# Kernel optimization log

Hardware: AMD Instinct MI355X
Metric: run time of the kernel (lower is better)

Reference implementation:

```python
import jax, jax.numpy as jnp
import numpy as np

B, T, C, NH = 1, 2048, 1024, 16
HS = C // NH            # 64
LEVEL = 6
LMIN = 2 ** LEVEL       # 64 (tail block size)
NB = T // LMIN          # 32 complete sets


def setup_inputs() -> dict:
    key = jax.random.key(0)
    ks = jax.random.split(key, 8)
    def w(k, shape, fan_in):
        return jax.random.normal(k, shape, jnp.float32) / np.sqrt(fan_in)
    return {
        "x": jax.random.normal(ks[0], (B, T, C), jnp.float32),
        "Wq": w(ks[1], (C, C), C),
        "Wk": w(ks[2], (C, C), C),
        "Wv": w(ks[3], (C, C), C),
        "Wkmap": w(ks[4], (HS, HS * HS), HS * HS),
        "bkmap": jnp.zeros((HS,), jnp.float32),
        "Wvmap": w(ks[5], (HS, HS * HS), HS * HS),
        "bvmap": jnp.zeros((HS,), jnp.float32),
        "Wc": w(ks[6], (C, C), C),
        "bc": jnp.zeros((C,), jnp.float32),
    }


def reference(x, Wq, Wk, Wv, Wkmap, bkmap, Wvmap, bvmap, Wc, bc):
    phi = lambda t: jax.nn.elu(t) + 1.0  # feature_map='elu'
    # preprocess: projections + feature map (no q/k normalization)
    q = phi((x @ Wq.T).reshape(B, T, NH, HS))
    k = phi((x @ Wk.T).reshape(B, T, NH, HS))
    v = (x @ Wv.T).reshape(B, T, NH, HS)

    # per-position outer products k_t (x) v_t, grouped into LMIN-sized blocks
    op = jnp.einsum('bthd,bthe->bthde', k, v).reshape(B, NB, LMIN, NH, HS, HS)
    # set feature = final state of linear-attn recurrence over each full block
    set_f = op.sum(axis=2).reshape(B, NB, NH, HS * HS)            # [B,NB,NH,HS^2]
    # tail feature at t = state over [t - t%LMIN, t] = in-block prefix cumsum
    tail_f = jnp.cumsum(op, axis=2).reshape(B, T, NH, HS * HS)    # [B,T,NH,HS^2]

    K = set_f @ Wkmap.T + bkmap      # [B,NB,NH,HS] (k_mapping=True)
    V = set_f @ Wvmap.T + bvmap      # [B,NB,NH,HS] (v_mapping=True)
    K_tail = tail_f @ Wkmap.T + bkmap  # [B,T,NH,HS]
    V_tail = tail_f @ Wvmap.T + bvmap  # [B,T,NH,HS]

    scale = 1.0 / np.sqrt(HS)
    logits = jnp.einsum('bthd,bshd->bhts', q, K) * scale          # [B,NH,T,NB]
    # query t may attend only complete sets strictly before its own block
    mask = jnp.arange(NB)[None, :] < (jnp.arange(T) // LMIN)[:, None]  # [T,NB]
    logits = jnp.where(mask[None, None], logits, -jnp.inf)
    tail_logit = (jnp.einsum('bthd,bthd->bth', q, K_tail) * scale)
    tail_logit = tail_logit.transpose(0, 2, 1)[..., None]         # [B,NH,T,1]

    att = jax.nn.softmax(jnp.concatenate([logits, tail_logit], axis=-1), axis=-1)
    out = (jnp.einsum('bhts,bshd->bhtd', att[..., :-1], V)
           + att[..., -1:] * V_tail.transpose(0, 2, 1, 3))        # [B,NH,T,HS]
    out = out.transpose(0, 2, 1, 3).reshape(B, T, C)
    return out @ Wc.T + bc
```

## Files before the change

kernel.cpp:

```cpp
#include <hip/hip_runtime.h>
#include <hip/hip_bf16.h>
#include <math.h>

typedef __hip_bfloat16 bf16;
typedef __attribute__((ext_vector_type(8))) short short8;
typedef __attribute__((ext_vector_type(4))) float f32x4;

#define C_DIM 1024
#define NHEAD 16
#define HS 64

__device__ __forceinline__ float bf2f(bf16 x) { return __bfloat162float(x); }

__device__ __forceinline__ void split8(const float* p, short8& h, short8& l) {
    float4 f0 = reinterpret_cast<const float4*>(p)[0];
    float4 f1 = reinterpret_cast<const float4*>(p)[1];
    float vals[8] = {f0.x, f0.y, f0.z, f0.w, f1.x, f1.y, f1.z, f1.w};
#pragma unroll
    for (int j = 0; j < 8; ++j) {
        bf16 hb = __float2bfloat16(vals[j]);
        float r = vals[j] - __bfloat162float(hb);
        h[j] = *reinterpret_cast<short*>(&hb);
        bf16 lb = __float2bfloat16(r);
        l[j] = *reinterpret_cast<short*>(&lb);
    }
}

__device__ __forceinline__ short8* tchunk(bf16* tile, int row, int ch) {
    return reinterpret_cast<short8*>(tile + row * 64 + (((ch) ^ (row & 7)) << 3));
}

__global__ __launch_bounds__(256) void presplit_all_kernel(
    const float* __restrict__ x, const float* __restrict__ Wq,
    const float* __restrict__ Wk, const float* __restrict__ Wv,
    bf16* __restrict__ xh, bf16* __restrict__ xl,
    bf16* __restrict__ wqh, bf16* __restrict__ wql,
    bf16* __restrict__ wkh, bf16* __restrict__ wkl,
    bf16* __restrict__ wvh, bf16* __restrict__ wvl)
{
    int blk = blockIdx.x;
    const float* src; bf16 *dh, *dl; long off;
    if (blk < 1024)      { src = x;  dh = xh;  dl = xl;  off = (long)blk * 2048; }
    else if (blk < 1536) { src = Wq; dh = wqh; dl = wql; off = (long)(blk - 1024) * 2048; }
    else if (blk < 2048) { src = Wk; dh = wkh; dl = wkl; off = (long)(blk - 1536) * 2048; }
    else                 { src = Wv; dh = wvh; dl = wvl; off = (long)(blk - 2048) * 2048; }
    long p = off + threadIdx.x * 8;
    short8 h8, l8;
    split8(&src[p], h8, l8);
    *reinterpret_cast<short8*>(&dh[p]) = h8;
    *reinterpret_cast<short8*>(&dl[p]) = l8;
}

__global__ __launch_bounds__(256) void presplit_wc_kernel(
    const float* __restrict__ Wc, bf16* __restrict__ wch, bf16* __restrict__ wcl)
{
    long p = (long)blockIdx.x * 2048 + threadIdx.x * 8;
    short8 h8, l8;
    split8(&Wc[p], h8, l8);
    *reinterpret_cast<short8*>(&wch[p]) = h8;
    *reinterpret_cast<short8*>(&wcl[p]) = l8;
}

__global__ __launch_bounds__(256) void presplit_wmap_kernel(
    const float* __restrict__ WK, const float* __restrict__ WV, bf16* __restrict__ Wm4)
{
    int d = blockIdx.x;
    int row = threadIdx.x >> 2, e0 = (threadIdx.x & 3) * 16;
    const float* pk = &WK[(long)row * 4096 + d * 64 + e0];
    const float* pv = &WV[(long)row * 4096 + d * 64 + e0];
    long bKh = (((long)(d * 4 + 0) * 64) + row) * 64 + e0;
    long bKl = (((long)(d * 4 + 1) * 64) + row) * 64 + e0;
    long bVh = (((long)(d * 4 + 2) * 64) + row) * 64 + e0;
    long bVl = (((long)(d * 4 + 3) * 64) + row) * 64 + e0;
    short8 h8, l8;
    split8(pk, h8, l8);     *(short8*)&Wm4[bKh] = h8;     *(short8*)&Wm4[bKl] = l8;
    split8(pk + 8, h8, l8); *(short8*)&Wm4[bKh + 8] = h8; *(short8*)&Wm4[bKl + 8] = l8;
    split8(pv, h8, l8);     *(short8*)&Wm4[bVh] = h8;     *(short8*)&Wm4[bVl] = l8;
    split8(pv + 8, h8, l8); *(short8*)&Wm4[bVh + 8] = h8; *(short8*)&Wm4[bVl + 8] = l8;
}

__global__ __launch_bounds__(256) void qkv_kernel(
    const bf16* __restrict__ xh, const bf16* __restrict__ xl,
    const bf16* __restrict__ wqh, const bf16* __restrict__ wql,
    const bf16* __restrict__ wkh, const bf16* __restrict__ wkl,
    const bf16* __restrict__ wvh, const bf16* __restrict__ wvl,
    float* __restrict__ qkv)
{
    __shared__ bf16 Ah[8192], Al[8192], Bh[8192], Bl[8192];
    const int tid = threadIdx.x;
    const int lane = tid & 63, wid = tid >> 6;
    const int wr = wid >> 1, wc = wid & 1;
    const int proj = blockIdx.x >> 3;
    const int n0 = (blockIdx.x & 7) * 128;
    const int m0 = blockIdx.y * 128;
    const bf16* Bhp = proj == 0 ? wqh : (proj == 1 ? wkh : wvh);
    const bf16* Blp = proj == 0 ? wql : (proj == 1 ? wkl : wvl);
    float* C = qkv + (long)proj * 2097152;

    f32x4 acc[4][4] = {};
    for (int kt = 0; kt < 16; ++kt) {
        const int k0 = kt << 6;
#pragma unroll
        for (int i = 0; i < 4; ++i) {
            int cc = tid + i * 256;
            int row = cc >> 3, ch = cc & 7;
            *tchunk(Ah, row, ch) = *(const short8*)&xh[(long)(m0 + row) * 1024 + k0 + ch * 8];
            *tchunk(Al, row, ch) = *(const short8*)&xl[(long)(m0 + row) * 1024 + k0 + ch * 8];
            *tchunk(Bh, row, ch) = *(const short8*)&Bhp[(long)(n0 + row) * 1024 + k0 + ch * 8];
            *tchunk(Bl, row, ch) = *(const short8*)&Blp[(long)(n0 + row) * 1024 + k0 + ch * 8];
        }
        __syncthreads();
#pragma unroll
        for (int kk = 0; kk < 2; ++kk) {
            short8 afh[4], afl[4], bfh[4], bfl[4];
#pragma unroll
            for (int t = 0; t < 4; ++t) {
                int ra = wr * 64 + t * 16 + (lane & 15);
                int rb = wc * 64 + t * 16 + (lane & 15);
                int ch = kk * 4 + (lane >> 4);
                afh[t] = *tchunk(Ah, ra, ch);
                afl[t] = *tchunk(Al, ra, ch);
                bfh[t] = *tchunk(Bh, rb, ch);
                bfl[t] = *tchunk(Bl, rb, ch);
            }
#pragma unroll
            for (int tm = 0; tm < 4; ++tm)
#pragma unroll
                for (int tn = 0; tn < 4; ++tn) {
                    acc[tm][tn] = __builtin_amdgcn_mfma_f32_16x16x32_bf16(
                        afh[tm], bfh[tn], acc[tm][tn], 0, 0, 0);
                    acc[tm][tn] = __builtin_amdgcn_mfma_f32_16x16x32_bf16(
                        afh[tm], bfl[tn], acc[tm][tn], 0, 0, 0);
                    acc[tm][tn] = __builtin_amdgcn_mfma_f32_16x16x32_bf16(
                        afl[tm], bfh[tn], acc[tm][tn], 0, 0, 0);
                }
        }
        __syncthreads();
    }
#pragma unroll
    for (int tm = 0; tm < 4; ++tm)
#pragma unroll
        for (int tn = 0; tn < 4; ++tn)
#pragma unroll
            for (int r = 0; r < 4; ++r) {
                int row = m0 + wr * 64 + tm * 16 + (lane >> 4) * 4 + r;
                int col = n0 + wc * 64 + tn * 16 + (lane & 15);
                float v = acc[tm][tn][r];
                if (proj < 2) v = v > 0.f ? v + 1.f : __expf(v);
                C[(long)row * 1024 + col] = v;
            }
}

__global__ __launch_bounds__(256) void setfeat_kernel(
    const float* __restrict__ kbuf, const float* __restrict__ vbuf,
    const bf16* __restrict__ Wm4,
    const float* __restrict__ bkmap, const float* __restrict__ bvmap,
    float* __restrict__ Ktail, float* __restrict__ Vtail,
    float* __restrict__ Kset, float* __restrict__ Vset)
{
    __shared__ char smem[49152];
    bf16* Wt = reinterpret_cast<bf16*>(smem);
    float* kT = reinterpret_cast<float*>(smem + 32768);
    float(*WallK)[64] = reinterpret_cast<float(*)[64]>(smem);
    float(*WallV)[64] = reinterpret_cast<float(*)[64]>(smem + 16384);

    const int tid = threadIdx.x;
    const int lane = tid & 63, wid = tid >> 6;
    const int wr = wid >> 1, wc = wid & 1;
    const int b = blockIdx.x >> 4, h = blockIdx.x & 15;
    const long base_kv = ((long)b * 64) * C_DIM + h * HS;

    {
        int s = tid >> 2, cg = tid & 3;
        const float* src = &kbuf[base_kv + (long)s * C_DIM + cg * 16];
        float f[16];
#pragma unroll
        for (int j = 0; j < 4; ++j)
            *reinterpret_cast<float4*>(&f[j * 4]) = reinterpret_cast<const float4*>(src)[j];
#pragma unroll
        for (int j = 0; j < 16; ++j)
            kT[(cg * 16 + j) * 64 + s] = f[j];
    }
    short8 vh[2][2], vl[2][2];
#pragma unroll
    for (int tm = 0; tm < 2; ++tm)
#pragma unroll
        for (int kk = 0; kk < 2; ++kk) {
            const float* vp = &vbuf[base_kv +
                (long)(wr * 32 + tm * 16 + (lane & 15)) * C_DIM + kk * 32 + (lane >> 4) * 8];
            split8(vp, vh[tm][kk], vl[tm][kk]);
        }
    f32x4 accK[2][2] = {}, accV[2][2] = {};
    __syncthreads();

    for (int d = 0; d < 64; ++d) {
#pragma unroll
        for (int i = 0; i < 8; ++i) {
            int cc = tid + i * 256;
            int part = cc >> 9, row = (cc >> 3) & 63, ch = cc & 7;
            *tchunk(Wt + part * 4096, row, ch) =
                *(const short8*)&Wm4[(((long)(d * 4 + part) * 64) + row) * 64 + ch * 8];
        }
        __syncthreads();
        f32x4 GK[2][2] = {}, GV[2][2] = {};
#pragma unroll
        for (int kk = 0; kk < 2; ++kk) {
            short8 bkh[2], bkl[2], bvh[2], bvl[2];
#pragma unroll
            for (int t = 0; t < 2; ++t) {
                int rb = wc * 32 + t * 16 + (lane & 15);
                int ch = kk * 4 + (lane >> 4);
                bkh[t] = *tchunk(Wt,         rb, ch);
                bkl[t] = *tchunk(Wt + 4096,  rb, ch);
                bvh[t] = *tchunk(Wt + 8192,  rb, ch);
                bvl[t] = *tchunk(Wt + 12288, rb, ch);
            }
#pragma unroll
            for (int tm = 0; tm < 2; ++tm)
#pragma unroll
                for (int tn = 0; tn < 2; ++tn) {
                    GK[tm][tn] = __builtin_amdgcn_mfma_f32_16x16x32_bf16(
                        vh[tm][kk], bkh[tn], GK[tm][tn], 0, 0, 0);
                    GK[tm][tn] = __builtin_amdgcn_mfma_f32_16x16x32_bf16(
                        vh[tm][kk], bkl[tn], GK[tm][tn], 0, 0, 0);
                    GK[tm][tn] = __builtin_amdgcn_mfma_f32_16x16x32_bf16(
                        vl[tm][kk], bkh[tn], GK[tm][tn], 0, 0, 0);
                    GV[tm][tn] = __builtin_amdgcn_mfma_f32_16x16x32_bf16(
                        vh[tm][kk], bvh[tn], GV[tm][tn], 0, 0, 0);
                    GV[tm][tn] = __builtin_amdgcn_mfma_f32_16x16x32_bf16(
                        vh[tm][kk], bvl[tn], GV[tm][tn], 0, 0, 0);
                    GV[tm][tn] = __builtin_amdgcn_mfma_f32_16x16x32_bf16(
                        vl[tm][kk], bvh[tn], GV[tm][tn], 0, 0, 0);
                }
        }
#pragma unroll
        for (int tm = 0; tm < 2; ++tm) {
            f32x4 kv = *reinterpret_cast<const f32x4*>(
                &kT[d * 64 + wr * 32 + tm * 16 + (lane >> 4) * 4]);
#pragma unroll
            for (int tn = 0; tn < 2; ++tn)
#pragma unroll
                for (int r = 0; r < 4; ++r) {
                    accK[tm][tn][r] += kv[r] * GK[tm][tn][r];
                    accV[tm][tn][r] += kv[r] * GV[tm][tn][r];
                }
        }
        __syncthreads();
    }
#pragma unroll
    for (int tm = 0; tm < 2; ++tm)
#pragma unroll
        for (int tn = 0; tn < 2; ++tn)
#pragma unroll
            for (int r = 0; r < 4; ++r) {
                int row = wr * 32 + tm * 16 + (lane >> 4) * 4 + r;
                int col = wc * 32 + tn * 16 + (lane & 15);
                WallK[row][col] = accK[tm][tn][r];
                WallV[row][col] = accV[tm][tn][r];
            }
    __syncthreads();
    if (tid < 128) {
        int i = tid & 63;
        bool isV = tid >= 64;
        const float bi = isV ? bvmap[i] : bkmap[i];
        float run = 0.f;
        for (int s = 0; s < 64; ++s) {
            run += isV ? WallV[s][i] : WallK[s][i];
            float val = run + bi;
            long t = (long)b * 64 + s;
            if (isV) Vtail[t * C_DIM + h * HS + i] = val;
            else     Ktail[t * C_DIM + h * HS + i] = val;
            if (s == 63) {
                if (isV) Vset[(b * NHEAD + h) * HS + i] = val;
                else     Kset[(b * NHEAD + h) * HS + i] = val;
            }
        }
    }
}

__global__ __launch_bounds__(256) void attn_kernel(
    const float* __restrict__ qbuf, const float* __restrict__ Kset,
    const float* __restrict__ Vset, const float* __restrict__ Ktail,
    const float* __restrict__ Vtail, bf16* __restrict__ atth, bf16* __restrict__ attl)
{
    __shared__ float qsh[4][64];
    __shared__ float attsh[4][64];
    const int tid = threadIdx.x, lane = tid & 63, wid = tid >> 6;
    const int g = blockIdx.x * 4 + wid;
    const int t = g >> 4, h = g & 15;
    const int nb = t >> 6;
    const float scale = 0.125f;
    const long qoff = (long)t * C_DIM + h * HS;
    qsh[wid][lane] = qbuf[qoff + lane];
    __syncthreads();
    float logit = -INFINITY;
    if (lane < nb) {
        float s = 0.f;
        const float* Kp = &Kset[(lane * NHEAD + h) * HS];
        for (int d = 0; d < 64; ++d) s += qsh[wid][d] * Kp[d];
        logit = s * scale;
    } else if (lane == nb) {
        float s = 0.f;
        const float* Kp = &Ktail[qoff];
        for (int d = 0; d < 64; ++d) s += qsh[wid][d] * Kp[d];
        logit = s * scale;
    }
    float m = logit;
    for (int off = 32; off; off >>= 1) m = fmaxf(m, __shfl_xor(m, off, 64));
    float e = (lane <= nb) ? __expf(logit - m) : 0.f;
    float sum = e;
    for (int off = 32; off; off >>= 1) sum += __shfl_xor(sum, off, 64);
    attsh[wid][lane] = e / sum;
    __syncthreads();
    float out = 0.f;
    for (int s = 0; s < nb; ++s)
        out += attsh[wid][s] * Vset[(s * NHEAD + h) * HS + lane];
    out += attsh[wid][nb] * Vtail[qoff + lane];
    bf16 hb = __float2bfloat16(out);
    atth[qoff + lane] = hb;
    attl[qoff + lane] = __float2bfloat16(out - bf2f(hb));
}

__global__ __launch_bounds__(256) void gemm_final_kernel(
    const bf16* __restrict__ ah, const bf16* __restrict__ al,
    const bf16* __restrict__ bh, const bf16* __restrict__ bl,
    const float* __restrict__ bias, float* __restrict__ C)
{
    __shared__ bf16 Ah[8192], Al[8192], Bh[4096], Bl[4096];
    const int tid = threadIdx.x;
    const int lane = tid & 63, wid = tid >> 6;
    const int wr = wid >> 1, wc = wid & 1;
    const int m0 = blockIdx.y * 128, n0 = blockIdx.x * 64;

    f32x4 acc[4][2] = {};
    for (int kt = 0; kt < 16; ++kt) {
        const int k0 = kt << 6;
#pragma unroll
        for (int i = 0; i < 4; ++i) {
            int cc = tid + i * 256;
            int row = cc >> 3, ch = cc & 7;
            *tchunk(Ah, row, ch) = *(const short8*)&ah[(long)(m0 + row) * 1024 + k0 + ch * 8];
            *tchunk(Al, row, ch) = *(const short8*)&al[(long)(m0 + row) * 1024 + k0 + ch * 8];
        }
#pragma unroll
        for (int i = 0; i < 2; ++i) {
            int cc = tid + i * 256;
            int row = cc >> 3, ch = cc & 7;
            *tchunk(Bh, row, ch) = *(const short8*)&bh[(long)(n0 + row) * 1024 + k0 + ch * 8];
            *tchunk(Bl, row, ch) = *(const short8*)&bl[(long)(n0 + row) * 1024 + k0 + ch * 8];
        }
        __syncthreads();
#pragma unroll
        for (int kk = 0; kk < 2; ++kk) {
            short8 afh[4], afl[4], bfh[2], bfl[2];
#pragma unroll
            for (int t = 0; t < 4; ++t) {
                int ra = wr * 64 + t * 16 + (lane & 15);
                int ch = kk * 4 + (lane >> 4);
                afh[t] = *tchunk(Ah, ra, ch);
                afl[t] = *tchunk(Al, ra, ch);
            }
#pragma unroll
            for (int t = 0; t < 2; ++t) {
                int rb = wc * 32 + t * 16 + (lane & 15);
                int ch = kk * 4 + (lane >> 4);
                bfh[t] = *tchunk(Bh, rb, ch);
                bfl[t] = *tchunk(Bl, rb, ch);
            }
#pragma unroll
            for (int tm = 0; tm < 4; ++tm)
#pragma unroll
                for (int tn = 0; tn < 2; ++tn) {
                    acc[tm][tn] = __builtin_amdgcn_mfma_f32_16x16x32_bf16(
                        afh[tm], bfh[tn], acc[tm][tn], 0, 0, 0);
                    acc[tm][tn] = __builtin_amdgcn_mfma_f32_16x16x32_bf16(
                        afh[tm], bfl[tn], acc[tm][tn], 0, 0, 0);
                    acc[tm][tn] = __builtin_amdgcn_mfma_f32_16x16x32_bf16(
                        afl[tm], bfh[tn], acc[tm][tn], 0, 0, 0);
                }
        }
        __syncthreads();
    }
#pragma unroll
    for (int tm = 0; tm < 4; ++tm)
#pragma unroll
        for (int tn = 0; tn < 2; ++tn)
#pragma unroll
            for (int r = 0; r < 4; ++r) {
                int row = m0 + wr * 64 + tm * 16 + (lane >> 4) * 4 + r;
                int col = n0 + wc * 32 + tn * 16 + (lane & 15);
                C[(long)row * 1024 + col] = acc[tm][tn][r] + bias[col];
            }
}

extern "C" void kernel_launch(void* const* d_in, const int* in_sizes, int n_in,
                              void* d_out, int out_size, void* d_ws, size_t ws_size,
                              hipStream_t stream)
{
    const float* x     = (const float*)d_in[0];
    const float* Wq    = (const float*)d_in[1];
    const float* Wk    = (const float*)d_in[2];
    const float* Wv    = (const float*)d_in[3];
    const float* Wkmap = (const float*)d_in[4];
    const float* bkmap = (const float*)d_in[5];
    const float* Wvmap = (const float*)d_in[6];
    const float* bvmap = (const float*)d_in[7];
    const float* Wc    = (const float*)d_in[8];
    const float* bc    = (const float*)d_in[9];
    float* out = (float*)d_out;

    char* ws = (char*)d_ws;
    const long MB = 1l << 20;
    float* q   = (float*)(ws + 0 * MB);
    float* k   = (float*)(ws + 8 * MB);
    float* v   = (float*)(ws + 16 * MB);
    bf16* xh   = (bf16*)(ws + 24 * MB);
    bf16* xl   = (bf16*)(ws + 28 * MB);
    bf16* wqh  = (bf16*)(ws + 32 * MB);
    bf16* wql  = (bf16*)(ws + 34 * MB);
    bf16* wkh  = (bf16*)(ws + 36 * MB);
    bf16* wkl  = (bf16*)(ws + 38 * MB);
    bf16* wvh  = (bf16*)(ws + 40 * MB);
    bf16* wvl  = (bf16*)(ws + 42 * MB);
    bf16* Wm4  = (bf16*)(ws + 44 * MB);
    float* Ktail = (float*)(ws + 24 * MB);
    float* Vtail = (float*)(ws + 32 * MB);
    float* Kset  = (float*)(ws + 40 * MB);
    float* Vset  = (float*)(ws + 41 * MB);
    bf16* atth   = (bf16*)(ws + 8 * MB);
    bf16* attl   = (bf16*)(ws + 12 * MB);
    bf16* wch    = (bf16*)(ws + 44 * MB);
    bf16* wcl    = (bf16*)(ws + 46 * MB);

    presplit_all_kernel<<<2560, 256, 0, stream>>>(x, Wq, Wk, Wv, xh, xl,
                                                  wqh, wql, wkh, wkl, wvh, wvl);
    presplit_wmap_kernel<<<64, 256, 0, stream>>>(Wkmap, Wvmap, Wm4);
    qkv_kernel<<<dim3(24, 16), 256, 0, stream>>>(xh, xl, wqh, wql, wkh, wkl,
                                                 wvh, wvl, q);
    setfeat_kernel<<<512, 256, 0, stream>>>(k, v, Wm4, bkmap, bvmap,
                                            Ktail, Vtail, Kset, Vset);
    presplit_wc_kernel<<<512, 256, 0, stream>>>(Wc, wch, wcl);
    attn_kernel<<<8192, 256, 0, stream>>>(q, Kset, Vset, Ktail, Vtail, atth, attl);
    gemm_final_kernel<<<dim3(16, 16), 256, 0, stream>>>(atth, attl, wch, wcl, bc, out);
}
```

Before: 304.0 us.

## Pre-swizzle bf16 operands in global memory and load tiles via global_load_lds

New measurement: 292.2 us. 3.9% less time.

```diff
diff --git a/kernel.cpp b/kernel.cpp
--- a/kernel.cpp
+++ b/kernel.cpp
@@ -11,6 +11,12 @@
 #define HS 64
 
 __device__ __forceinline__ float bf2f(bf16 x) { return __bfloat162float(x); }
+
+__device__ __forceinline__ void gl16(const void* g, void* l) {
+    __builtin_amdgcn_global_load_lds(
+        (const __attribute__((address_space(1))) unsigned int*)g,
+        (__attribute__((address_space(3))) unsigned int*)l, 16, 0, 0);
+}
 
 __device__ __forceinline__ void split8(const float* p, short8& h, short8& l) {
     float4 f0 = reinterpret_cast<const float4*>(p)[0];
@@ -45,20 +51,24 @@
     else if (blk < 2048) { src = Wk; dh = wkh; dl = wkl; off = (long)(blk - 1536) * 2048; }
     else                 { src = Wv; dh = wvh; dl = wvl; off = (long)(blk - 2048) * 2048; }
     long p = off + threadIdx.x * 8;
+    int j = (int)(((p >> 3) ^ (p >> 10)) & 7);
+    long dp = (p & ~56l) | ((long)j << 3);
     short8 h8, l8;
     split8(&src[p], h8, l8);
-    *reinterpret_cast<short8*>(&dh[p]) = h8;
-    *reinterpret_cast<short8*>(&dl[p]) = l8;
+    *reinterpret_cast<short8*>(&dh[dp]) = h8;
+    *reinterpret_cast<short8*>(&dl[dp]) = l8;
 }
 
 __global__ __launch_bounds__(256) void presplit_wc_kernel(
     const float* __restrict__ Wc, bf16* __restrict__ wch, bf16* __restrict__ wcl)
 {
     long p = (long)blockIdx.x * 2048 + threadIdx.x * 8;
+    int j = (int)(((p >> 3) ^ (p >> 10)) & 7);
+    long dp = (p & ~56l) | ((long)j << 3);
     short8 h8, l8;
     split8(&Wc[p], h8, l8);
-    *reinterpret_cast<short8*>(&wch[p]) = h8;
-    *reinterpret_cast<short8*>(&wcl[p]) = l8;
+    *reinterpret_cast<short8*>(&wch[dp]) = h8;
+    *reinterpret_cast<short8*>(&wcl[dp]) = l8;
 }
 
 __global__ __launch_bounds__(256) void presplit_wmap_kernel(
@@ -66,17 +76,19 @@
 {
     int d = blockIdx.x;
     int row = threadIdx.x >> 2, e0 = (threadIdx.x & 3) * 16;
+    int sw0 = (((e0 >> 3) + 0) ^ (row & 7)) & 7;
+    int sw1 = (((e0 >> 3) + 1) ^ (row & 7)) & 7;
     const float* pk = &WK[(long)row * 4096 + d * 64 + e0];
     const float* pv = &WV[(long)row * 4096 + d * 64 + e0];
-    long bKh = (((long)(d * 4 + 0) * 64) + row) * 64 + e0;
-    long bKl = (((long)(d * 4 + 1) * 64) + row) * 64 + e0;
-    long bVh = (((long)(d * 4 + 2) * 64) + row) * 64 + e0;
-    long bVl = (((long)(d * 4 + 3) * 64) + row) * 64 + e0;
+    long bKh = ((long)(d * 4 + 0) * 64 + row) * 64;
+    long bKl = ((long)(d * 4 + 1) * 64 + row) * 64;
+    long bVh = ((long)(d * 4 + 2) * 64 + row) * 64;
+    long bVl = ((long)(d * 4 + 3) * 64 + row) * 64;
     short8 h8, l8;
-    split8(pk, h8, l8);     *(short8*)&Wm4[bKh] = h8;     *(short8*)&Wm4[bKl] = l8;
-    split8(pk + 8, h8, l8); *(short8*)&Wm4[bKh + 8] = h8; *(short8*)&Wm4[bKl + 8] = l8;
-    split8(pv, h8, l8);     *(short8*)&Wm4[bVh] = h8;     *(short8*)&Wm4[bVl] = l8;
-    split8(pv + 8, h8, l8); *(short8*)&Wm4[bVh + 8] = h8; *(short8*)&Wm4[bVl + 8] = l8;
+    split8(pk, h8, l8);     *(short8*)&Wm4[bKh + sw0*8] = h8; *(short8*)&Wm4[bKl + sw0*8] = l8;
+    split8(pk + 8, h8, l8); *(short8*)&Wm4[bKh + sw1*8] = h8; *(short8*)&Wm4[bKl + sw1*8] = l8;
+    split8(pv, h8, l8);     *(short8*)&Wm4[bVh + sw0*8] = h8; *(short8*)&Wm4[bVl + sw0*8] = l8;
+    split8(pv + 8, h8, l8); *(short8*)&Wm4[bVh + sw1*8] = h8; *(short8*)&Wm4[bVl + sw1*8] = l8;
 }
 
 __global__ __launch_bounds__(256) void qkv_kernel(
@@ -86,7 +98,7 @@
     const bf16* __restrict__ wvh, const bf16* __restrict__ wvl,
     float* __restrict__ qkv)
 {
-    __shared__ bf16 Ah[8192], Al[8192], Bh[8192], Bl[8192];
+    __shared__ bf16 lds[32768];
     const int tid = threadIdx.x;
     const int lane = tid & 63, wid = tid >> 6;
     const int wr = wid >> 1, wc = wid & 1;
@@ -96,6 +108,7 @@
     const bf16* Bhp = proj == 0 ? wqh : (proj == 1 ? wkh : wvh);
     const bf16* Blp = proj == 0 ? wql : (proj == 1 ? wkl : wvl);
     float* C = qkv + (long)proj * 2097152;
+    char* lb = reinterpret_cast<char*>(lds);
 
     f32x4 acc[4][4] = {};
     for (int kt = 0; kt < 16; ++kt) {
@@ -103,11 +116,13 @@
 #pragma unroll
         for (int i = 0; i < 4; ++i) {
             int cc = tid + i * 256;
-            int row = cc >> 3, ch = cc & 7;
-            *tchunk(Ah, row, ch) = *(const short8*)&xh[(long)(m0 + row) * 1024 + k0 + ch * 8];
-            *tchunk(Al, row, ch) = *(const short8*)&xl[(long)(m0 + row) * 1024 + k0 + ch * 8];
-            *tchunk(Bh, row, ch) = *(const short8*)&Bhp[(long)(n0 + row) * 1024 + k0 + ch * 8];
-            *tchunk(Bl, row, ch) = *(const short8*)&Blp[(long)(n0 + row) * 1024 + k0 + ch * 8];
+            int row = cc >> 3, j = cc & 7;
+            long soA = (long)(m0 + row) * 1024 + k0 + j * 8;
+            long soB = (long)(n0 + row) * 1024 + k0 + j * 8;
+            gl16(&xh[soA],  lb + cc * 16);
+            gl16(&xl[soA],  lb + 16384 + cc * 16);
+            gl16(&Bhp[soB], lb + 32768 + cc * 16);
+            gl16(&Blp[soB], lb + 49152 + cc * 16);
         }
         __syncthreads();
 #pragma unroll
@@ -118,10 +133,10 @@
                 int ra = wr * 64 + t * 16 + (lane & 15);
                 int rb = wc * 64 + t * 16 + (lane & 15);
                 int ch = kk * 4 + (lane >> 4);
-                afh[t] = *tchunk(Ah, ra, ch);
-                afl[t] = *tchunk(Al, ra, ch);
-                bfh[t] = *tchunk(Bh, rb, ch);
-                bfl[t] = *tchunk(Bl, rb, ch);
+                afh[t] = *tchunk(lds, ra, ch);
+                afl[t] = *tchunk(lds + 8192, ra, ch);
+                bfh[t] = *tchunk(lds + 16384, rb, ch);
+                bfl[t] = *tchunk(lds + 24576, rb, ch);
             }
 #pragma unroll
             for (int tm = 0; tm < 4; ++tm)
@@ -151,27 +166,27 @@
             }
 }
 
-__global__ __launch_bounds__(256) void setfeat_kernel(
+__global__ __launch_bounds__(512) void setfeat_kernel(
     const float* __restrict__ kbuf, const float* __restrict__ vbuf,
     const bf16* __restrict__ Wm4,
     const float* __restrict__ bkmap, const float* __restrict__ bvmap,
     float* __restrict__ Ktail, float* __restrict__ Vtail,
     float* __restrict__ Kset, float* __restrict__ Vset)
 {
-    __shared__ char smem[49152];
+    __shared__ char smem[65536];
     bf16* Wt = reinterpret_cast<bf16*>(smem);
-    float* kT = reinterpret_cast<float*>(smem + 32768);
-    float(*WallK)[64] = reinterpret_cast<float(*)[64]>(smem);
-    float(*WallV)[64] = reinterpret_cast<float(*)[64]>(smem + 16384);
-
     const int tid = threadIdx.x;
-    const int lane = tid & 63, wid = tid >> 6;
+    const int grp = tid >> 8;
+    const int tl = tid & 255;
+    const int lane = tl & 63, wid = tl >> 6;
     const int wr = wid >> 1, wc = wid & 1;
-    const int b = blockIdx.x >> 4, h = blockIdx.x & 15;
+    const int pairIdx = blockIdx.x * 2 + grp;
+    const int b = pairIdx >> 4, h = pairIdx & 15;
     const long base_kv = ((long)b * 64) * C_DIM + h * HS;
+    float* kT = reinterpret_cast<float*>(smem + 32768 + grp * 16384);
 
     {
-        int s = tid >> 2, cg = tid & 3;
+        int s = tl >> 2, cg = tl & 3;
         const float* src = &kbuf[base_kv + (long)s * C_DIM + cg * 16];
         float f[16];
 #pragma unroll
@@ -195,11 +210,9 @@
 
     for (int d = 0; d < 64; ++d) {
 #pragma unroll
-        for (int i = 0; i < 8; ++i) {
-            int cc = tid + i * 256;
-            int part = cc >> 9, row = (cc >> 3) & 63, ch = cc & 7;
-            *tchunk(Wt + part * 4096, row, ch) =
-                *(const short8*)&Wm4[(((long)(d * 4 + part) * 64) + row) * 64 + ch * 8];
+        for (int i = 0; i < 4; ++i) {
+            int cc = tid + i * 512;
+            gl16(&Wm4[(long)d * 16384 + (long)cc * 8], smem + (long)cc * 16);
         }
         __syncthreads();
         f32x4 GK[2][2] = {}, GV[2][2] = {};
@@ -247,6 +260,8 @@
         }
         __syncthreads();
     }
+    float(*WallK)[64] = reinterpret_cast<float(*)[64]>(smem + grp * 32768);
+    float(*WallV)[64] = reinterpret_cast<float(*)[64]>(smem + grp * 32768 + 16384);
 #pragma unroll
     for (int tm = 0; tm < 2; ++tm)
 #pragma unroll
@@ -259,9 +274,9 @@
                 WallV[row][col] = accV[tm][tn][r];
             }
     __syncthreads();
-    if (tid < 128) {
-        int i = tid & 63;
-        bool isV = tid >= 64;
+    if (tl < 128) {
+        int i = tl & 63;
+        bool isV = tl >= 64;
         const float bi = isV ? bvmap[i] : bkmap[i];
         float run = 0.f;
         for (int s = 0; s < 64; ++s) {
@@ -317,8 +332,10 @@
         out += attsh[wid][s] * Vset[(s * NHEAD + h) * HS + lane];
     out += attsh[wid][nb] * Vtail[qoff + lane];
     bf16 hb = __float2bfloat16(out);
-    atth[qoff + lane] = hb;
-    attl[qoff + lane] = __float2bfloat16(out - bf2f(hb));
+    int csw = (((lane >> 3) ^ (t & 7)) << 3) | (lane & 7);
+    long po = (long)t * 1024 + h * 64 + csw;
+    atth[po] = hb;
+    attl[po] = __float2bfloat16(out - bf2f(hb));
 }
 
 __global__ __launch_bounds__(256) void gemm_final_kernel(
@@ -326,11 +343,12 @@
     const bf16* __restrict__ bh, const bf16* __restrict__ bl,
     const float* __restrict__ bias, float* __restrict__ C)
 {
-    __shared__ bf16 Ah[8192], Al[8192], Bh[4096], Bl[4096];
+    __shared__ bf16 lds[24576];
     const int tid = threadIdx.x;
     const int lane = tid & 63, wid = tid >> 6;
     const int wr = wid >> 1, wc = wid & 1;
     const int m0 = blockIdx.y * 128, n0 = blockIdx.x * 64;
+    char* lb = reinterpret_cast<char*>(lds);
 
     f32x4 acc[4][2] = {};
     for (int kt = 0; kt < 16; ++kt) {
@@ -338,16 +356,18 @@
 #pragma unroll
         for (int i = 0; i < 4; ++i) {
             int cc = tid + i * 256;
-            int row = cc >> 3, ch = cc & 7;
-            *tchunk(Ah, row, ch) = *(const short8*)&ah[(long)(m0 + row) * 1024 + k0 + ch * 8];
-            *tchunk(Al, row, ch) = *(const short8*)&al[(long)(m0 + row) * 1024 + k0 + ch * 8];
+            int row = cc >> 3, j = cc & 7;
+            long so = (long)(m0 + row) * 1024 + k0 + j * 8;
+            gl16(&ah[so], lb + cc * 16);
+            gl16(&al[so], lb + 16384 + cc * 16);
         }
 #pragma unroll
         for (int i = 0; i < 2; ++i) {
             int cc = tid + i * 256;
-            int row = cc >> 3, ch = cc & 7;
-            *tchunk(Bh, row, ch) = *(const short8*)&bh[(long)(n0 + row) * 1024 + k0 + ch * 8];
-            *tchunk(Bl, row, ch) = *(const short8*)&bl[(long)(n0 + row) * 1024 + k0 + ch * 8];
+            int row = cc >> 3, j = cc & 7;
+            long so = (long)(n0 + row) * 1024 + k0 + j * 8;
+            gl16(&bh[so], lb + 32768 + cc * 16);
+            gl16(&bl[so], lb + 40960 + cc * 16);
         }
         __syncthreads();
 #pragma unroll
@@ -357,15 +377,15 @@
             for (int t = 0; t < 4; ++t) {
                 int ra = wr * 64 + t * 16 + (lane & 15);
                 int ch = kk * 4 + (lane >> 4);
-                afh[t] = *tchunk(Ah, ra, ch);
-                afl[t] = *tchunk(Al, ra, ch);
+                afh[t] = *tchunk(lds, ra, ch);
+                afl[t] = *tchunk(lds + 8192, ra, ch);
             }
 #pragma unroll
             for (int t = 0; t < 2; ++t) {
                 int rb = wc * 32 + t * 16 + (lane & 15);
                 int ch = kk * 4 + (lane >> 4);
-                bfh[t] = *tchunk(Bh, rb, ch);
-                bfl[t] = *tchunk(Bl, rb, ch);
+                bfh[t] = *tchunk(lds + 16384, rb, ch);
+                bfl[t] = *tchunk(lds + 20480, rb, ch);
             }
 #pragma unroll
             for (int tm = 0; tm < 4; ++tm)
@@ -437,7 +457,7 @@
     presplit_wmap_kernel<<<64, 256, 0, stream>>>(Wkmap, Wvmap, Wm4);
     qkv_kernel<<<dim3(24, 16), 256, 0, stream>>>(xh, xl, wqh, wql, wkh, wkl,
                                                  wvh, wvl, q);
-    setfeat_kernel<<<512, 256, 0, stream>>>(k, v, Wm4, bkmap, bvmap,
+    setfeat_kernel<<<256, 512, 0, stream>>>(k, v, Wm4, bkmap, bvmap,
                                             Ktail, Vtail, Kset, Vset);
     presplit_wc_kernel<<<512, 256, 0, stream>>>(Wc, wch, wcl);
     attn_kernel<<<8192, 256, 0, stream>>>(q, Kset, Vset, Ktail, Vtail, atth, attl);
```
